# Kernel tuning notes

Hardware: AMD Instinct MI355X
Metric: run time of the kernel (lower is better)

The kernel has to match this reference:

```python
import jax, jax.numpy as jnp
import numpy as np

C = 128
NUM_GROUPS = 32  # min(32, 128 // 4)
EPS = 1e-6


def group_norm(x, gamma, beta):
    N, Cc, H, W = x.shape
    xg = x.reshape(N, NUM_GROUPS, -1)
    mean = xg.mean(axis=-1, keepdims=True)
    var = ((xg - mean) ** 2).mean(axis=-1, keepdims=True)
    xn = ((xg - mean) * jax.lax.rsqrt(var + EPS)).reshape(N, Cc, H, W)
    return xn * gamma[None, :, None, None] + beta[None, :, None, None]


def conv1x1(x, w, b):
    # w: [C_out, C_in], b: [C_out]; 1x1 conv == channel matmul
    return jnp.einsum('nchw,oc->nohw', x, w) + b[None, :, None, None]


def setup_inputs() -> dict:
    key = jax.random.key(0)
    ks = jax.random.split(key, 11)
    s = 1.0 / np.sqrt(C)
    return {
        'x': jax.random.normal(ks[0], (4, C, 64, 64), dtype=jnp.float32),
        'gamma': jnp.ones((C,), jnp.float32),
        'beta': jnp.zeros((C,), jnp.float32),
        'wq': jax.random.normal(ks[1], (C, C), jnp.float32) * s,
        'bq': jnp.zeros((C,), jnp.float32),
        'wk': jax.random.normal(ks[2], (C, C), jnp.float32) * s,
        'bk': jnp.zeros((C,), jnp.float32),
        'wv': jax.random.normal(ks[3], (C, C), jnp.float32) * s,
        'bv': jnp.zeros((C,), jnp.float32),
        'wo': jax.random.normal(ks[4], (C, C), jnp.float32) * s,
        'bo': jnp.zeros((C,), jnp.float32),
    }


def reference(x, gamma, beta, wq, bq, wk, bk, wv, bv, wo, bo):
    N, Cc, H, W = x.shape
    L = H * W
    xn = group_norm(x, gamma, beta)
    q = conv1x1(xn, wq, bq).reshape(N, Cc, L)  # [N,C,L]
    k = conv1x1(xn, wk, bk).reshape(N, Cc, L)
    v = conv1x1(xn, wv, bv).reshape(N, Cc, L)
    scale = 1.0 / jnp.sqrt(jnp.asarray(Cc, x.dtype))
    scores = jnp.einsum('ncl,ncm->nlm', q, k) * scale  # [N,L,L]
    weights = jax.nn.softmax(scores, axis=-1)
    attn = jnp.einsum('nlm,ncm->ncl', weights, v).reshape(N, Cc, H, W)
    return x + conv1x1(attn, wo, bo)
```

## Files before the change

### kernel.cpp

```cpp
#include <hip/hip_runtime.h>
#include <hip/hip_bf16.h>


#define N_B 4
#define C_D 128
#define L_D 4096
#define SPLIT 4
#define KVB 64
#define FSTEPS ((L_D/SPLIT)/KVB)
#define QSCALE (0.08838834764831845f * 1.4426950408889634f)
#define FIXM 16.0f

using f32x4  = __attribute__((ext_vector_type(4))) float;
using f32x16 = __attribute__((ext_vector_type(16))) float;
using bf16x8 = __attribute__((ext_vector_type(8))) short;

static __device__ __forceinline__ unsigned short f2bf(float f){
  return (unsigned short)((__builtin_bit_cast(unsigned int, f) + 0x8000u) >> 16);
}
static __device__ __forceinline__ float bf2f(unsigned short u){
  unsigned int x = ((unsigned int)u) << 16;
  return __builtin_bit_cast(float, x);
}
static __device__ __forceinline__ unsigned int pk2(float a, float b){
  unsigned int ua = __builtin_bit_cast(unsigned int, a) + 0x8000u;
  unsigned int ub = __builtin_bit_cast(unsigned int, b) + 0x8000u;
  return __builtin_amdgcn_perm(ub, ua, 0x07060302u);
}
static __device__ __forceinline__ float exp2a(float x){
  float r; asm("v_exp_f32 %0, %1" : "=v"(r) : "v"(x)); return r;
}
static __device__ __forceinline__ void gll16(const void* g, void* l){
  __builtin_amdgcn_global_load_lds(
      (const __attribute__((address_space(1))) unsigned int*)g,
      (__attribute__((address_space(3))) unsigned int*)l, 16, 0, 0);
}

__global__ __launch_bounds__(256) void gnw_k(
    const float* __restrict__ x, float* __restrict__ stats,
    const float* __restrict__ wq, const float* __restrict__ wk,
    const float* __restrict__ wv, const float* __restrict__ wo,
    unsigned short* __restrict__ wbf)
{
  int b = blockIdx.x, t = threadIdx.x;
  if (b >= 128){
    int b2 = b - 128;
    int mat = b2 >> 4;
    const float* src = (mat == 0) ? wq : (mat == 1) ? wk : (mat == 2) ? wv : wo;
    int off = (b2 & 15) * 1024 + t * 4;
    float4 v = *(const float4*)(src + off);
    *(uint2*)(wbf + mat*16384 + off) = make_uint2(pk2(v.x, v.y), pk2(v.z, v.w));
    return;
  }
  const float4* p = (const float4*)(x + (size_t)b * (4 * L_D));
  float s = 0.f, ss = 0.f;
#pragma unroll
  for (int i = 0; i < 16; ++i){
    float4 v = p[t + i*256];
    s  += v.x + v.y + v.z + v.w;
    ss += v.x*v.x + v.y*v.y + v.z*v.z + v.w*v.w;
  }
#pragma unroll
  for (int off = 32; off > 0; off >>= 1){
    s  += __shfl_down(s, off);
    ss += __shfl_down(ss, off);
  }
  __shared__ float rs4[4], rss4[4];
  if ((t & 63) == 0){ rs4[t>>6] = s; rss4[t>>6] = ss; }
  __syncthreads();
  if (t == 0){
    s  = rs4[0]+rs4[1]+rs4[2]+rs4[3];
    ss = rss4[0]+rss4[1]+rss4[2]+rss4[3];
    float mean = s * (1.f/16384.f);
    float var  = ss * (1.f/16384.f) - mean*mean;
    if (var < 0.f) var = 0.f;
    stats[2*b]   = mean;
    stats[2*b+1] = rsqrtf(var + 1e-6f);
  }
}

__global__ __launch_bounds__(256) void qkv_k(
    const float* __restrict__ x, const float* __restrict__ stats,
    const float* __restrict__ gamma, const float* __restrict__ beta,
    const unsigned short* __restrict__ wbf,
    const float* __restrict__ bq, const float* __restrict__ bk,
    const float* __restrict__ bv,
    unsigned short* __restrict__ q_ws, unsigned short* __restrict__ k_ws,
    unsigned short* __restrict__ v_ws)
{
  __shared__ unsigned short xnT[64][136];
  __shared__ unsigned short qbuf[64][136];

  int t = threadIdx.x, b = blockIdx.x;
  int wi = b >> 8;
  int bt = b & 255;
  int n = bt >> 6, l0 = (bt & 63) * 64;

  {
    int l = t & 63, cq = t >> 6;
#pragma unroll
    for (int it = 0; it < 8; ++it){
      int c0 = cq*4 + it*16;
      int g  = c0 >> 2;
      float mean = stats[(n*32+g)*2];
      float rstd = stats[(n*32+g)*2+1];
      float vv[4];
#pragma unroll
      for (int jj = 0; jj < 4; ++jj){
        int c = c0 + jj;
        float sc = rstd * gamma[c];
        float bs = beta[c] - mean * sc;
        vv[jj] = x[(size_t)(n*C_D + c)*L_D + l0 + l]*sc + bs;
      }
      *(unsigned int*)&xnT[l][c0]   = pk2(vv[0], vv[1]);
      *(unsigned int*)&xnT[l][c0+2] = pk2(vv[2], vv[3]);
    }
  }
  __syncthreads();

  int w = t >> 6, lane = t & 63, u = lane >> 4, l15 = lane & 15;
  int wc = w >> 1, wl = w & 1;
  const unsigned short* W = wbf + wi*16384;
  const float* Bv = (wi == 0) ? bq : (wi == 1) ? bk : bv;

  f32x4 zz = {0.f,0.f,0.f,0.f};
  f32x4 acc[4][2];
#pragma unroll
  for (int ct = 0; ct < 4; ++ct)
#pragma unroll
    for (int lt = 0; lt < 2; ++lt) acc[ct][lt] = zz;

#pragma unroll
  for (int kst = 0; kst < 4; ++kst){
    bf16x8 bfrag[2];
#pragma unroll
    for (int lt = 0; lt < 2; ++lt)
      bfrag[lt] = *(const bf16x8*)&xnT[32*wl + 16*lt + l15][kst*32 + 8*u];
#pragma unroll
    for (int ct = 0; ct < 4; ++ct){
      bf16x8 af = *(const bf16x8*)(W + (size_t)(64*wc + 16*ct + l15)*C_D + kst*32 + 8*u);
#pragma unroll
      for (int lt = 0; lt < 2; ++lt)
        acc[ct][lt] = __builtin_amdgcn_mfma_f32_16x16x32_bf16(af, bfrag[lt], acc[ct][lt], 0, 0, 0);
    }
  }

  if (wi < 2){
    float qs = (wi == 0) ? QSCALE : 1.0f;
#pragma unroll
    for (int ct = 0; ct < 4; ++ct){
      float bias[4];
#pragma unroll
      for (int r = 0; r < 4; ++r) bias[r] = Bv[64*wc + 16*ct + 4*u + r];
#pragma unroll
      for (int lt = 0; lt < 2; ++lt){
        float v0 = (acc[ct][lt][0] + bias[0]) * qs;
        float v1 = (acc[ct][lt][1] + bias[1]) * qs;
        float v2 = (acc[ct][lt][2] + bias[2]) * qs;
        float v3 = (acc[ct][lt][3] + bias[3]) * qs;
        int row = 32*wl + 16*lt + l15;
        int col = 64*wc + 16*ct + 4*u;
        *(unsigned int*)&qbuf[row][col]   = pk2(v0, v1);
        *(unsigned int*)&qbuf[row][col+2] = pk2(v2, v3);
      }
    }
    __syncthreads();
    {
      int l = t >> 2, ch = t & 3;
      unsigned short* dst = ((wi == 0) ? q_ws : k_ws) + (size_t)(n*L_D + l0 + l)*C_D + ch*32;
#pragma unroll
      for (int i = 0; i < 4; ++i)
        *(uint4*)(dst + i*8) = *(const uint4*)&qbuf[l][ch*32 + i*8];
    }
  } else {
    int p16 = (l15 & 3) | ((l15 & 4) << 1) | ((l15 & 8) >> 1);
#pragma unroll
    for (int ct = 0; ct < 4; ++ct){
      float bias[4];
#pragma unroll
      for (int r = 0; r < 4; ++r) bias[r] = Bv[64*wc + 16*ct + 4*u + r];
#pragma unroll
      for (int lt = 0; lt < 2; ++lt)
#pragma unroll
        for (int r = 0; r < 4; ++r){
          int co = 64*wc + 16*ct + 4*u + r;
          v_ws[(size_t)(n*C_D + co)*L_D + l0 + 32*wl + 16*lt + p16] =
              f2bf(acc[ct][lt][r] + bias[r]);
        }
    }
  }
}

#define STEPBODY(STEP, SIN0, SIN1, SOUT0, SOUT1, DOQK)                           \
  {                                                                              \
    const int step_ = (STEP);                                                    \
    int pfi = step_ + 2; if (pfi > FSTEPS-1) pfi = FSTEPS-1;                     \
    int pbb = (step_ + 2) & 3;                                                   \
    {                                                                            \
      char* kN = shmem + (pbb << 14);                                            \
      char* vN = shmem + 65536 + (pbb << 14);                                    \
      gll16(kg[0] + (size_t)pfi*KVB*C_D, kN + ldof[0]);                          \
      gll16(kg[1] + (size_t)pfi*KVB*C_D, kN + ldof[1]);                          \
      gll16(vg[0] + pfi*KVB, vN + ldof[0]);                                      \
      gll16(vg[1] + pfi*KVB, vN + ldof[1]);                                      \
    }                                                                            \
    char* kB = shmem + ((step_ & 3) << 14);                                      \
    char* vP = shmem + 65536 + (((step_ - 1) & 3) << 14);                        \
    const bool doQK = (DOQK);                                                    \
    float p0[16], p1[16];                                                        \
    union Wu { unsigned int u[8]; bf16x8 h[2]; } Wm0, Wm1;                       \
    __builtin_amdgcn_s_setprio(1);                                               \
                                  \
    if (doQK){                                                                   \
      bf16x8 afr[8];                                                             \
      _Pragma("unroll")                                                          \
      for (int k = 0; k < 8; ++k)                                                \
        afr[k] = *(const bf16x8*)(kB + l31*256 +                                 \
                   ((32*k + 16*hi) ^ ((l31 & 15) << 4)));                        \
      SOUT0 = zz16;                                                              \
      _Pragma("unroll")                                                          \
      for (int k = 0; k < 8; ++k){                                               \
        SOUT0 = __builtin_amdgcn_mfma_f32_32x32x16_bf16(afr[k], qf[k], SOUT0, 0, 0, 0); \
        p0[2*k]   = exp2a(SIN0[2*k]   - FIXM);                                   \
        p0[2*k+1] = exp2a(SIN0[2*k+1] - FIXM);                                   \
      }                                                                          \
    } else {                                                                     \
      _Pragma("unroll")                                                          \
      for (int r = 0; r < 16; ++r) p0[r] = exp2a(SIN0[r] - FIXM);                \
    }                                                                            \
                                     \
    if (doQK){                                                                   \
      bf16x8 afr[8];                                                             \
      _Pragma("unroll")                                                          \
      for (int k = 0; k < 8; ++k)                                                \
        afr[k] = *(const bf16x8*)(kB + (32 + l31)*256 +                          \
                   ((32*k + 16*hi) ^ ((l31 & 15) << 4)));                        \
      SOUT1 = zz16;                                                              \
      _Pragma("unroll")                                                          \
      for (int k = 0; k < 8; ++k){                                               \
        SOUT1 = __builtin_amdgcn_mfma_f32_32x32x16_bf16(afr[k], qf[k], SOUT1, 0, 0, 0); \
        Wm0.u[k] = pk2(p0[2*k], p0[2*k+1]);                                      \
      }                                                                          \
    } else {                                                                     \
      _Pragma("unroll")                                                          \
      for (int k = 0; k < 8; ++k) Wm0.u[k] = pk2(p0[2*k], p0[2*k+1]);            \
    }                                                                            \
    rsum += (((p0[0]+p0[1])+(p0[2]+p0[3])) + ((p0[4]+p0[5])+(p0[6]+p0[7])))      \
          + (((p0[8]+p0[9])+(p0[10]+p0[11])) + ((p0[12]+p0[13])+(p0[14]+p0[15])));\
                                \
    _Pragma("unroll")                                                            \
    for (int sl = 0; sl < 2; ++sl){                                              \
      bf16x8 pfv = Wm0.h[sl];                                                    \
      bf16x8 vfr[4];                                                             \
      _Pragma("unroll")                                                          \
      for (int ct = 0; ct < 4; ++ct){                                            \
        int c = 32*ct + l31, vrow = c & 63;                                      \
        int lb = ((c >> 6) << 7) + 32*sl + 16*hi;                                \
        vfr[ct] = *(const bf16x8*)(vP + vrow*256 + (lb ^ ((vrow & 15) << 4)));   \
      }                                                                          \
      _Pragma("unroll")                                                          \
      for (int ct = 0; ct < 4; ++ct){                                            \
        accO[ct] = __builtin_amdgcn_mfma_f32_32x32x16_bf16(vfr[ct], pfv, accO[ct], 0, 0, 0); \
        p1[8*sl + 2*ct]     = exp2a(SIN1[8*sl + 2*ct]     - FIXM);               \
        p1[8*sl + 2*ct + 1] = exp2a(SIN1[8*sl + 2*ct + 1] - FIXM);               \
      }                                                                          \
    }                                                                            \
    _Pragma("unroll")                                                            \
    for (int k = 0; k < 8; ++k) Wm1.u[k] = pk2(p1[2*k], p1[2*k+1]);              \
    rsum += (((p1[0]+p1[1])+(p1[2]+p1[3])) + ((p1[4]+p1[5])+(p1[6]+p1[7])))      \
          + (((p1[8]+p1[9])+(p1[10]+p1[11])) + ((p1[12]+p1[13])+(p1[14]+p1[15])));\
                                                            \
    _Pragma("unroll")                                                            \
    for (int sl = 2; sl < 4; ++sl){                                              \
      bf16x8 pfv = Wm1.h[sl & 1];                                                \
      bf16x8 vfr[4];                                                             \
      _Pragma("unroll")                                                          \
      for (int ct = 0; ct < 4; ++ct){                                            \
        int c = 32*ct + l31, vrow = c & 63;                                      \
        int lb = ((c >> 6) << 7) + 32*sl + 16*hi;                                \
        vfr[ct] = *(const bf16x8*)(vP + vrow*256 + (lb ^ ((vrow & 15) << 4)));   \
      }                                                                          \
      _Pragma("unroll")                                                          \
      for (int ct = 0; ct < 4; ++ct)                                             \
        accO[ct] = __builtin_amdgcn_mfma_f32_32x32x16_bf16(vfr[ct], pfv, accO[ct], 0, 0, 0); \
    }                                                                            \
    __builtin_amdgcn_s_setprio(0);                                               \
    asm volatile("s_waitcnt vmcnt(4)" ::: "memory");                             \
    __builtin_amdgcn_s_barrier();                                                \
    asm volatile("" ::: "memory");                                               \
  }

__global__ __launch_bounds__(512, 2) void flash_split_k(
    const unsigned short* __restrict__ q_ws, const unsigned short* __restrict__ k_ws,
    const unsigned short* __restrict__ v_ws,
    unsigned short* __restrict__ po_ws, float* __restrict__ md_ws)
{
  __shared__ __align__(16) char shmem[131072];

  int t = threadIdx.x;
  int phys = blockIdx.x;
  int xcd = phys & 7, j = phys >> 3;
  int pair = xcd*8 + (j & 7);
  int s = j >> 3;
  int n = pair >> 4, lt256 = pair & 15;
  int l0 = lt256 * 256;
  int m_base = s * (L_D / SPLIT);
  int w = t >> 6, lane = t & 63, hi = lane >> 5, l31 = lane & 31;
  int lr = lane >> 4, ls = lane & 15;

  bf16x8 qf[8];
  {
    const unsigned short* qrow = q_ws + ((size_t)(n*L_D + l0 + 32*w + l31))*C_D;
#pragma unroll
    for (int kst = 0; kst < 8; ++kst)
      qf[kst] = *(const bf16x8*)(qrow + 16*kst + 8*hi);
  }

  f32x16 zz16;
#pragma unroll
  for (int i = 0; i < 16; ++i) zz16[i] = 0.f;
  f32x16 accO[4];
#pragma unroll
  for (int ct = 0; ct < 4; ++ct) accO[ct] = zz16;
  float rsum = 0.f;

  const unsigned short* kg[2];
  const unsigned short* vg[2];
  int ldof[2];
#pragma unroll
  for (int i = 0; i < 2; ++i){
    int row = 8*w + 4*i + lr;
    int ub = (ls << 4) ^ ((row & 15) << 4);
    kg[i] = k_ws + ((size_t)(n*L_D + m_base + row))*C_D + (ub >> 1);
    int c    = row + ((ub >> 7) << 6);
    int mloc = (ub & 127) >> 1;
    vg[i] = v_ws + ((size_t)(n*C_D + c))*L_D + m_base + mloc;
    ldof[i] = (8*w + 4*i)*256;
  }

#pragma unroll
  for (int pre = 0; pre < 3; ++pre){
    char* kD = shmem + (pre << 14);
    char* vD = shmem + 65536 + (pre << 14);
    gll16(kg[0] + (size_t)pre*KVB*C_D, kD + ldof[0]);
    gll16(kg[1] + (size_t)pre*KVB*C_D, kD + ldof[1]);
    gll16(vg[0] + pre*KVB, vD + ldof[0]);
    gll16(vg[1] + pre*KVB, vD + ldof[1]);
  }
  asm volatile("s_waitcnt vmcnt(4)" ::: "memory");
  __builtin_amdgcn_s_barrier();
  asm volatile("" ::: "memory");

  f32x16 sA0, sA1, sB0, sB1;
  {
    __builtin_amdgcn_s_setprio(1);
    sA0 = zz16; sA1 = zz16;
    bf16x8 afr[8];
#pragma unroll
    for (int k = 0; k < 8; ++k)
      afr[k] = *(const bf16x8*)(shmem + l31*256 + ((32*k + 16*hi) ^ ((l31 & 15) << 4)));
#pragma unroll
    for (int k = 0; k < 8; ++k)
      sA0 = __builtin_amdgcn_mfma_f32_32x32x16_bf16(afr[k], qf[k], sA0, 0, 0, 0);
#pragma unroll
    for (int k = 0; k < 8; ++k)
      afr[k] = *(const bf16x8*)(shmem + (32 + l31)*256 + ((32*k + 16*hi) ^ ((l31 & 15) << 4)));
#pragma unroll
    for (int k = 0; k < 8; ++k)
      sA1 = __builtin_amdgcn_mfma_f32_32x32x16_bf16(afr[k], qf[k], sA1, 0, 0, 0);
    __builtin_amdgcn_s_setprio(0);
  }

  for (int e = 1; e < 17; e += 2){
    STEPBODY(e,     sA0, sA1, sB0, sB1, true)
    STEPBODY(e + 1, sB0, sB1, sA0, sA1, (e + 1 < FSTEPS))
  }

  asm volatile("s_waitcnt vmcnt(0)" ::: "memory");
  __builtin_amdgcn_s_barrier();
  asm volatile("" ::: "memory");

  rsum += __shfl_xor(rsum, 32);

  char* tB = shmem;
  {
    int lloc = 32*w + l31;
    int tsw = (lloc & 15) << 4;
    char* tr = tB + (size_t)lloc*256;
#pragma unroll
    for (int ct = 0; ct < 4; ++ct)
#pragma unroll
      for (int q = 0; q < 4; ++q){
        int cb2 = 64*ct + 16*q + 8*hi;
        *(unsigned int*)(tr + ((cb2    ) ^ tsw)) = pk2(accO[ct][4*q+0], accO[ct][4*q+1]);
        *(unsigned int*)(tr + ((cb2 + 4) ^ tsw)) = pk2(accO[ct][4*q+2], accO[ct][4*q+3]);
      }
  }
  __syncthreads();
  {
    int row2 = t >> 1, hf2 = t & 1;
    int tile = row2 >> 7, lrow = row2 & 127;
    size_t pb = ((size_t)((n*32 + 2*lt256 + tile)*SPLIT + s)) * (size_t)(128*128);
    unsigned short* dst = po_ws + pb + (size_t)lrow*128 + hf2*64;
    const char* srcr = tB + row2*256;
    int sw2 = (row2 & 15) << 4;
#pragma unroll
    for (int i = 0; i < 8; ++i)
      *(uint4*)(dst + 8*i) = *(const uint4*)(srcr + ((hf2*128 + 16*i) ^ sw2));
  }
  if (lane < 32){
    int lg = 32*w + lane;
    int tile2 = lg >> 7, lrow2 = lg & 127;
    size_t mb2 = ((size_t)((n*32 + 2*lt256 + tile2)*SPLIT + s)) * 128;
    md_ws[mb2 + lrow2] = rsum;
  }
}

__global__ __launch_bounds__(256) void combine_k(
    const unsigned short* __restrict__ po_ws, const float* __restrict__ md_ws,
    const float* __restrict__ x, const unsigned short* __restrict__ wo_bf,
    const float* __restrict__ bo, float* __restrict__ out)
{
  __shared__ __align__(16) char aB[16384];

  int t = threadIdx.x, b = blockIdx.x;
  int xcd = b & 7, j = b >> 3;
  int pair = xcd*8 + (j & 7);
  int quarter = j >> 3;
  int n = pair >> 4, lt256 = pair & 15;
  int lt64 = lt256*4 + quarter;
  int f = lt64 >> 1, loff = (lt64 & 1)*64, l0 = lt64*64;
  size_t pbase = ((size_t)((n*32 + f)*SPLIT)) * (size_t)(128*128);
  size_t mbase = ((size_t)((n*32 + f)*SPLIT)) * 128;

  {
    int l = t >> 2, q = t & 3;
    float Dg = 0.f;
#pragma unroll
    for (int s2 = 0; s2 < SPLIT; ++s2)
      Dg += md_ws[mbase + s2*128 + loff + l];
    float inv = 1.0f / Dg;

    float a[32];
#pragma unroll
    for (int i = 0; i < 32; ++i) a[i] = 0.f;
#pragma unroll
    for (int s2 = 0; s2 < SPLIT; ++s2){
      const uint4* p = (const uint4*)(po_ws + pbase + (size_t)s2*(128*128)
                                      + (size_t)(loff + l)*128 + q*32);
#pragma unroll
      for (int i = 0; i < 4; ++i){
        uint4 uv = p[i];
        unsigned int uu[4] = {uv.x, uv.y, uv.z, uv.w};
#pragma unroll
        for (int j2 = 0; j2 < 4; ++j2){
          a[8*i + 2*j2]     += bf2f((unsigned short)(uu[j2] & 0xffffu));
          a[8*i + 2*j2 + 1] += bf2f((unsigned short)(uu[j2] >> 16));
        }
      }
    }
    char* ar = aB + l*256;
    int asw = (l & 7) << 4;
#pragma unroll
    for (int i = 0; i < 16; ++i){
      int cb = q*64 + 4*i;
      *(unsigned int*)(ar + (cb ^ asw)) = pk2(a[2*i]*inv, a[2*i+1]*inv);
    }
  }
  __syncthreads();

  int w = t >> 6, lane = t & 63, hi = lane >> 5, l31 = lane & 31;
  int lh = w >> 1, ch = w & 1;
  f32x16 acc[2];
#pragma unroll
  for (int ci = 0; ci < 2; ++ci)
#pragma unroll
    for (int i = 0; i < 16; ++i) acc[ci][i] = 0.f;

#pragma unroll
  for (int kst = 0; kst < 8; ++kst){
    int row = 32*lh + l31;
    bf16x8 bfg = *(const bf16x8*)(aB + row*256 + ((32*kst + 16*hi) ^ ((row & 7) << 4)));
#pragma unroll
    for (int ci = 0; ci < 2; ++ci){
      bf16x8 af = *(const bf16x8*)(wo_bf + (size_t)(64*ch + 32*ci + l31)*C_D + 16*kst + 8*hi);
      acc[ci] = __builtin_amdgcn_mfma_f32_32x32x16_bf16(af, bfg, acc[ci], 0, 0, 0);
    }
  }
#pragma unroll
  for (int ci = 0; ci < 2; ++ci)
#pragma unroll
    for (int r = 0; r < 16; ++r){
      int o = 64*ch + 32*ci + (r & 3) + 8*(r >> 2) + 4*hi;
      size_t idx = (size_t)(n*C_D + o)*L_D + l0 + 32*lh + l31;
      out[idx] = x[idx] + bo[o] + acc[ci][r];
    }
}

extern "C" void kernel_launch(void* const* d_in, const int* in_sizes, int n_in,
                              void* d_out, int out_size, void* d_ws, size_t ws_size,
                              hipStream_t stream) {
  const float* x     = (const float*)d_in[0];
  const float* gamma = (const float*)d_in[1];
  const float* beta  = (const float*)d_in[2];
  const float* wq    = (const float*)d_in[3];
  const float* bq    = (const float*)d_in[4];
  const float* wk    = (const float*)d_in[5];
  const float* bk    = (const float*)d_in[6];
  const float* wv    = (const float*)d_in[7];
  const float* bv    = (const float*)d_in[8];
  const float* wo    = (const float*)d_in[9];
  const float* bo    = (const float*)d_in[10];
  float* out = (float*)d_out;

  char* ws = (char*)d_ws;
  float* stats          = (float*)ws;
  unsigned short* q_ws  = (unsigned short*)(ws + 4096);
  unsigned short* k_ws  = q_ws + (size_t)N_B * L_D * C_D;
  unsigned short* v_ws  = k_ws + (size_t)N_B * L_D * C_D;
  unsigned short* po_ws = v_ws + (size_t)N_B * L_D * C_D;
  float* md_ws          = (float*)(po_ws + (size_t)N_B * 32 * SPLIT * 128 * 128);
  unsigned short* wbf   = (unsigned short*)(md_ws + (size_t)N_B * 32 * SPLIT * 128);

  gnw_k<<<192, 256, 0, stream>>>(x, stats, wq, wk, wv, wo, wbf);
  qkv_k<<<768, 256, 0, stream>>>(x, stats, gamma, beta, wbf, bq, bk, bv,
                                 q_ws, k_ws, v_ws);
  flash_split_k<<<256, 512, 0, stream>>>(q_ws, k_ws, v_ws, po_ws, md_ws);
  combine_k<<<256, 256, 0, stream>>>(po_ws, md_ws, x, wbf + 3*16384, bo, out);
}
```

Measured before the change: 73.74 us.

## Compute Q/K/V in one block per tile; halve combine tile size

The QKV projection kernel now loops over the three weight matrices inside each block, so the normalized input tile is loaded and staged in shared memory once instead of three times. The grid drops from 768 to 256 blocks. The combine kernel now processes 32-row tiles with one 32x32 output chunk per wave, doubling its grid to 512 blocks for more parallelism. The trade-offs are less parallelism and a longer serial loop in the QKV kernel, an extra barrier per projection, and more blocks each re-reading the Wo weights in combine.

```diff
diff --git a/kernel.cpp b/kernel.cpp
--- a/kernel.cpp
+++ b/kernel.cpp
@@ -92,9 +92,7 @@
   __shared__ unsigned short qbuf[64][136];
 
   int t = threadIdx.x, b = blockIdx.x;
-  int wi = b >> 8;
-  int bt = b & 255;
-  int n = bt >> 6, l0 = (bt & 63) * 64;
+  int n = b >> 6, l0 = (b & 63) * 64;
 
   {
     int l = t & 63, cq = t >> 6;
@@ -120,73 +118,77 @@
 
   int w = t >> 6, lane = t & 63, u = lane >> 4, l15 = lane & 15;
   int wc = w >> 1, wl = w & 1;
-  const unsigned short* W = wbf + wi*16384;
-  const float* Bv = (wi == 0) ? bq : (wi == 1) ? bk : bv;
-
   f32x4 zz = {0.f,0.f,0.f,0.f};
-  f32x4 acc[4][2];
-#pragma unroll
-  for (int ct = 0; ct < 4; ++ct)
-#pragma unroll
-    for (int lt = 0; lt < 2; ++lt) acc[ct][lt] = zz;
-
-#pragma unroll
-  for (int kst = 0; kst < 4; ++kst){
-    bf16x8 bfrag[2];
-#pragma unroll
-    for (int lt = 0; lt < 2; ++lt)
-      bfrag[lt] = *(const bf16x8*)&xnT[32*wl + 16*lt + l15][kst*32 + 8*u];
-#pragma unroll
-    for (int ct = 0; ct < 4; ++ct){
-      bf16x8 af = *(const bf16x8*)(W + (size_t)(64*wc + 16*ct + l15)*C_D + kst*32 + 8*u);
+
+  for (int wi = 0; wi < 3; ++wi){
+    const unsigned short* W = wbf + wi*16384;
+    const float* Bv = (wi == 0) ? bq : (wi == 1) ? bk : bv;
+
+    f32x4 acc[4][2];
+#pragma unroll
+    for (int ct = 0; ct < 4; ++ct)
+#pragma unroll
+      for (int lt = 0; lt < 2; ++lt) acc[ct][lt] = zz;
+
+#pragma unroll
+    for (int kst = 0; kst < 4; ++kst){
+      bf16x8 bfrag[2];
 #pragma unroll
       for (int lt = 0; lt < 2; ++lt)
-        acc[ct][lt] = __builtin_amdgcn_mfma_f32_16x16x32_bf16(af, bfrag[lt], acc[ct][lt], 0, 0, 0);
+        bfrag[lt] = *(const bf16x8*)&xnT[32*wl + 16*lt + l15][kst*32 + 8*u];
+#pragma unroll
+      for (int ct = 0; ct < 4; ++ct){
+        bf16x8 af = *(const bf16x8*)(W + (size_t)(64*wc + 16*ct + l15)*C_D + kst*32 + 8*u);
+#pragma unroll
+        for (int lt = 0; lt < 2; ++lt)
+          acc[ct][lt] = __builtin_amdgcn_mfma_f32_16x16x32_bf16(af, bfrag[lt], acc[ct][lt], 0, 0, 0);
+      }
     }
-  }
-
-  if (wi < 2){
-    float qs = (wi == 0) ? QSCALE : 1.0f;
-#pragma unroll
-    for (int ct = 0; ct < 4; ++ct){
-      float bias[4];
-#pragma unroll
-      for (int r = 0; r < 4; ++r) bias[r] = Bv[64*wc + 16*ct + 4*u + r];
-#pragma unroll
-      for (int lt = 0; lt < 2; ++lt){
-        float v0 = (acc[ct][lt][0] + bias[0]) * qs;
-        float v1 = (acc[ct][lt][1] + bias[1]) * qs;
-        float v2 = (acc[ct][lt][2] + bias[2]) * qs;
-        float v3 = (acc[ct][lt][3] + bias[3]) * qs;
-        int row = 32*wl + 16*lt + l15;
-        int col = 64*wc + 16*ct + 4*u;
-        *(unsigned int*)&qbuf[row][col]   = pk2(v0, v1);
-        *(unsigned int*)&qbuf[row][col+2] = pk2(v2, v3);
-      }
-    }
-    __syncthreads();
-    {
-      int l = t >> 2, ch = t & 3;
-      unsigned short* dst = ((wi == 0) ? q_ws : k_ws) + (size_t)(n*L_D + l0 + l)*C_D + ch*32;
-#pragma unroll
-      for (int i = 0; i < 4; ++i)
-        *(uint4*)(dst + i*8) = *(const uint4*)&qbuf[l][ch*32 + i*8];
-    }
-  } else {
-    int p16 = (l15 & 3) | ((l15 & 4) << 1) | ((l15 & 8) >> 1);
-#pragma unroll
-    for (int ct = 0; ct < 4; ++ct){
-      float bias[4];
-#pragma unroll
-      for (int r = 0; r < 4; ++r) bias[r] = Bv[64*wc + 16*ct + 4*u + r];
-#pragma unroll
-      for (int lt = 0; lt < 2; ++lt)
-#pragma unroll
-        for (int r = 0; r < 4; ++r){
-          int co = 64*wc + 16*ct + 4*u + r;
-          v_ws[(size_t)(n*C_D + co)*L_D + l0 + 32*wl + 16*lt + p16] =
-              f2bf(acc[ct][lt][r] + bias[r]);
+
+    if (wi < 2){
+      float qs = (wi == 0) ? QSCALE : 1.0f;
+      __syncthreads();
+#pragma unroll
+      for (int ct = 0; ct < 4; ++ct){
+        float bias[4];
+#pragma unroll
+        for (int r = 0; r < 4; ++r) bias[r] = Bv[64*wc + 16*ct + 4*u + r];
+#pragma unroll
+        for (int lt = 0; lt < 2; ++lt){
+          float v0 = (acc[ct][lt][0] + bias[0]) * qs;
+          float v1 = (acc[ct][lt][1] + bias[1]) * qs;
+          float v2 = (acc[ct][lt][2] + bias[2]) * qs;
+          float v3 = (acc[ct][lt][3] + bias[3]) * qs;
+          int row = 32*wl + 16*lt + l15;
+          int col = 64*wc + 16*ct + 4*u;
+          *(unsigned int*)&qbuf[row][col]   = pk2(v0, v1);
+          *(unsigned int*)&qbuf[row][col+2] = pk2(v2, v3);
         }
+      }
+      __syncthreads();
+      {
+        int l = t >> 2, ch = t & 3;
+        unsigned short* dst = ((wi == 0) ? q_ws : k_ws) + (size_t)(n*L_D + l0 + l)*C_D + ch*32;
+#pragma unroll
+        for (int i = 0; i < 4; ++i)
+          *(uint4*)(dst + i*8) = *(const uint4*)&qbuf[l][ch*32 + i*8];
+      }
+    } else {
+      int p16 = (l15 & 3) | ((l15 & 4) << 1) | ((l15 & 8) >> 1);
+#pragma unroll
+      for (int ct = 0; ct < 4; ++ct){
+        float bias[4];
+#pragma unroll
+        for (int r = 0; r < 4; ++r) bias[r] = Bv[64*wc + 16*ct + 4*u + r];
+#pragma unroll
+        for (int lt = 0; lt < 2; ++lt)
+#pragma unroll
+          for (int r = 0; r < 4; ++r){
+            int co = 64*wc + 16*ct + 4*u + r;
+            v_ws[(size_t)(n*C_D + co)*L_D + l0 + 32*wl + 16*lt + p16] =
+                f2bf(acc[ct][lt][r] + bias[r]);
+          }
+      }
     }
   }
 }
@@ -421,35 +423,37 @@
     const float* __restrict__ x, const unsigned short* __restrict__ wo_bf,
     const float* __restrict__ bo, float* __restrict__ out)
 {
-  __shared__ __align__(16) char aB[16384];
+  __shared__ __align__(16) char aB[8192];
 
   int t = threadIdx.x, b = blockIdx.x;
   int xcd = b & 7, j = b >> 3;
   int pair = xcd*8 + (j & 7);
-  int quarter = j >> 3;
+  int eighth = j >> 3;
   int n = pair >> 4, lt256 = pair & 15;
-  int lt64 = lt256*4 + quarter;
-  int f = lt64 >> 1, loff = (lt64 & 1)*64, l0 = lt64*64;
+  int lt32 = lt256*8 + eighth;
+  int f = lt32 >> 2;
+  int loff = (lt32 & 3) * 32;
+  int l0 = lt32 * 32;
   size_t pbase = ((size_t)((n*32 + f)*SPLIT)) * (size_t)(128*128);
   size_t mbase = ((size_t)((n*32 + f)*SPLIT)) * 128;
 
   {
-    int l = t >> 2, q = t & 3;
+    int l = t >> 3, q8 = t & 7;
     float Dg = 0.f;
 #pragma unroll
     for (int s2 = 0; s2 < SPLIT; ++s2)
       Dg += md_ws[mbase + s2*128 + loff + l];
     float inv = 1.0f / Dg;
 
-    float a[32];
-#pragma unroll
-    for (int i = 0; i < 32; ++i) a[i] = 0.f;
+    float a[16];
+#pragma unroll
+    for (int i = 0; i < 16; ++i) a[i] = 0.f;
 #pragma unroll
     for (int s2 = 0; s2 < SPLIT; ++s2){
       const uint4* p = (const uint4*)(po_ws + pbase + (size_t)s2*(128*128)
-                                      + (size_t)(loff + l)*128 + q*32);
-#pragma unroll
-      for (int i = 0; i < 4; ++i){
+                                      + (size_t)(loff + l)*128 + q8*16);
+#pragma unroll
+      for (int i = 0; i < 2; ++i){
         uint4 uv = p[i];
         unsigned int uu[4] = {uv.x, uv.y, uv.z, uv.w};
 #pragma unroll
@@ -462,39 +466,30 @@
     char* ar = aB + l*256;
     int asw = (l & 7) << 4;
 #pragma unroll
-    for (int i = 0; i < 16; ++i){
-      int cb = q*64 + 4*i;
+    for (int i = 0; i < 8; ++i){
+      int cb = q8*32 + 4*i;
       *(unsigned int*)(ar + (cb ^ asw)) = pk2(a[2*i]*inv, a[2*i+1]*inv);
     }
   }
   __syncthreads();
 
   int w = t >> 6, lane = t & 63, hi = lane >> 5, l31 = lane & 31;
-  int lh = w >> 1, ch = w & 1;
-  f32x16 acc[2];
-#pragma unroll
-  for (int ci = 0; ci < 2; ++ci)
-#pragma unroll
-    for (int i = 0; i < 16; ++i) acc[ci][i] = 0.f;
+  f32x16 acc;
+#pragma unroll
+  for (int i = 0; i < 16; ++i) acc[i] = 0.f;
 
 #pragma unroll
   for (int kst = 0; kst < 8; ++kst){
-    int row = 32*lh + l31;
-    bf16x8 bfg = *(const bf16x8*)(aB + row*256 + ((32*kst + 16*hi) ^ ((row & 7) << 4)));
-#pragma unroll
-    for (int ci = 0; ci < 2; ++ci){
-      bf16x8 af = *(const bf16x8*)(wo_bf + (size_t)(64*ch + 32*ci + l31)*C_D + 16*kst + 8*hi);
-      acc[ci] = __builtin_amdgcn_mfma_f32_32x32x16_bf16(af, bfg, acc[ci], 0, 0, 0);
-    }
-  }
-#pragma unroll
-  for (int ci = 0; ci < 2; ++ci)
-#pragma unroll
-    for (int r = 0; r < 16; ++r){
-      int o = 64*ch + 32*ci + (r & 3) + 8*(r >> 2) + 4*hi;
-      size_t idx = (size_t)(n*C_D + o)*L_D + l0 + 32*lh + l31;
-      out[idx] = x[idx] + bo[o] + acc[ci][r];
-    }
+    bf16x8 bfg = *(const bf16x8*)(aB + l31*256 + ((32*kst + 16*hi) ^ ((l31 & 7) << 4)));
+    bf16x8 af = *(const bf16x8*)(wo_bf + (size_t)(32*w + l31)*C_D + 16*kst + 8*hi);
+    acc = __builtin_amdgcn_mfma_f32_32x32x16_bf16(af, bfg, acc, 0, 0, 0);
+  }
+#pragma unroll
+  for (int r = 0; r < 16; ++r){
+    int o = 32*w + (r & 3) + 8*(r >> 2) + 4*hi;
+    size_t idx = (size_t)(n*C_D + o)*L_D + l0 + l31;
+    out[idx] = x[idx] + bo[o] + acc[r];
+  }
 }
 
 extern "C" void kernel_launch(void* const* d_in, const int* in_sizes, int n_in,
@@ -523,8 +518,8 @@
   unsigned short* wbf   = (unsigned short*)(md_ws + (size_t)N_B * 32 * SPLIT * 128);
 
   gnw_k<<<192, 256, 0, stream>>>(x, stats, wq, wk, wv, wo, wbf);
-  qkv_k<<<768, 256, 0, stream>>>(x, stats, gamma, beta, wbf, bq, bk, bv,
+  qkv_k<<<256, 256, 0, stream>>>(x, stats, gamma, beta, wbf, bq, bk, bv,
                                  q_ws, k_ws, v_ws);
   flash_split_k<<<256, 512, 0, stream>>>(q_ws, k_ws, v_ws, po_ws, md_ws);
-  combine_k<<<256, 256, 0, stream>>>(po_ws, md_ws, x, wbf + 3*16384, bo, out);
-}
+  combine_k<<<512, 256, 0, stream>>>(po_ws, md_ws, x, wbf + 3*16384, bo, out);
+}
```

Result: no change. 72.71 us (-1.4%).
